# Kernel optimization log

Measured on AMD Instinct MI355X. Metric: run time of the kernel, lower is better.

The kernel has to match this reference:

```python
import jax, jax.numpy as jnp
import numpy as np

N_NODES = 50000
N_EDGES = 1600000
DIM_IN = 128
DIM_OUT = 128
EPS = 1e-10


def setup_inputs() -> dict:
    key = jax.random.key(0)
    k1, k2, k3, k4, k5 = jax.random.split(key, 5)
    feat_in = jax.random.normal(k1, (N_NODES, DIM_IN), dtype=jnp.float32)
    rows = jax.random.randint(k2, (N_EDGES,), 0, N_NODES, dtype=jnp.int32)
    cols = jax.random.randint(k3, (N_EDGES,), 0, N_NODES, dtype=jnp.int32)
    # normalized adjacency values (positive, ~1/deg scale)
    vals = jax.random.uniform(k4, (N_EDGES,), dtype=jnp.float32) / 32.0
    W = jax.random.normal(k5, (DIM_OUT, DIM_IN), dtype=jnp.float32) * 0.05
    b = jnp.zeros((DIM_OUT,), dtype=jnp.float32)
    scale = jnp.ones((DIM_OUT,), dtype=jnp.float32)
    offset = jnp.zeros((DIM_OUT,), dtype=jnp.float32)
    return {"feat_in": feat_in, "rows": rows, "cols": cols, "vals": vals,
            "W": W, "b": b, "scale": scale, "offset": offset}


def reference(feat_in, rows, cols, vals, W, b, scale, offset):
    # torch.sparse.mm(adj_norm, feat_in): gather source features, scale by
    # edge value, scatter-add into destination rows.
    msgs = vals[:, None] * feat_in[cols]                       # [E, D_in]
    feat_aggr = jax.ops.segment_sum(msgs, rows, num_segments=N_NODES)  # [N, D_in]
    # f_lin (nn.Linear): x @ W.T + b
    feat_trans = feat_aggr @ W.T + b                           # [N, D_out]
    # act = ReLU
    a = jax.nn.relu(feat_trans)
    # f_norm: per-row (feature-dim) normalization, biased variance
    mean = jnp.mean(a, axis=1, keepdims=True)
    var = jnp.mean((a - mean) ** 2, axis=1, keepdims=True) + EPS
    feat_out = (a - mean) * scale * jax.lax.rsqrt(var) + offset
    return feat_out
```

## Files before the change

kernel.cpp:

```cpp
#include <hip/hip_runtime.h>

typedef unsigned int uint;
typedef unsigned short ushort;
typedef __attribute__((ext_vector_type(8))) short short8;
typedef __attribute__((ext_vector_type(4))) float floatx4;

#define N_NODES 50000
#define N_EDGES 1600000
#define DIM 128
#define LN_EPS 1e-10f

#define ROWS_PER_BUCKET 64
#define N_BUCKETS 782
#define BUCKET_CAP 2560
#define EPB 6250
#define SB 256
#define FCB 1563
#define CAPR 76

__device__ __forceinline__ uint f2bf(float x) {
    uint u = __float_as_uint(x);
    return (u + 0x7FFFu + ((u >> 16) & 1u)) >> 16;
}

__global__ __launch_bounds__(1024) void prep(
    const float* __restrict__ feat, const float* __restrict__ W,
    const int* __restrict__ rows, const int* __restrict__ cols,
    const float* __restrict__ vals, int* __restrict__ gcnt,
    int2* __restrict__ perm, uint* __restrict__ featb_u,
    ushort* __restrict__ wbf)
{
    __shared__ int  cnt[N_BUCKETS];
    __shared__ int  gbase[N_BUCKETS];
    __shared__ int  lbase[N_BUCKETS];
    __shared__ int  csum[64];
    __shared__ uint stash[EPB];
    __shared__ int2 stageE[EPB];
    const int bx = blockIdx.x;
    const int t  = threadIdx.x;

    if (bx >= SB) {
        int cb = bx - SB;
        if (cb < FCB) {
            int i = cb * 1024 + t;
            if (i < N_NODES * DIM / 4) {
                float4 v = ((const float4*)feat)[i];
                ((uint2*)featb_u)[i] = make_uint2(
                    f2bf(v.x) | (f2bf(v.y) << 16),
                    f2bf(v.z) | (f2bf(v.w) << 16));
            }
        } else {
            for (int idx = t; idx < DIM * DIM; idx += 1024)
                wbf[idx] = (ushort)f2bf(W[idx]);
        }
        return;
    }

    for (int i = t; i < N_BUCKETS; i += 1024) cnt[i] = 0;
    __syncthreads();
    const int base = bx * EPB;
    for (int k = t; k < EPB; k += 1024) {
        int r = rows[base + k];
        int rank = atomicAdd(&cnt[r >> 6], 1);
        stash[k] = ((uint)rank << 16) | (uint)r;
    }
    __syncthreads();

    for (int i = t; i < N_BUCKETS; i += 1024) {
        int c = cnt[i];
        gbase[i] = c ? atomicAdd(&gcnt[i], c) : 0;
    }
    if (t < 64) {
        int s = 0;
        for (int j = 0; j < 13; ++j) {
            int idx = t * 13 + j;
            if (idx < N_BUCKETS) s += cnt[idx];
        }
        csum[t] = s;
    }
    __syncthreads();
    if (t == 0) {
        int s = 0;
        for (int i = 0; i < 64; ++i) { int c = csum[i]; csum[i] = s; s += c; }
    }
    __syncthreads();
    if (t < 64) {
        int run = csum[t];
        for (int j = 0; j < 13; ++j) {
            int idx = t * 13 + j;
            if (idx < N_BUCKETS) { lbase[idx] = run; run += cnt[idx]; }
        }
    }
    __syncthreads();

    for (int k = t; k < EPB; k += 1024) {
        int e = base + k;
        uint s = stash[k];
        int r = (int)(s & 0xFFFFu);
        int rank = (int)(s >> 16);
        int b = r >> 6;
        int pos = lbase[b] + rank;
        stageE[pos] = make_int2(
            (uint)cols[e] | ((uint)(r & 63) << 16) | ((uint)b << 22),
            __float_as_int(vals[e]));
    }
    __syncthreads();

    for (int j = t; j < EPB; j += 1024) {
        int2 p = stageE[j];
        uint b = ((uint)p.x) >> 22;
        int pos = gbase[b] + (j - lbase[b]);
        if (pos < BUCKET_CAP)
            perm[(size_t)b * BUCKET_CAP + pos] = p;
    }
}

__global__ __launch_bounds__(512, 6) void agg_fused(
    const int2* __restrict__ perm, const int* __restrict__ gcnt,
    const ushort* __restrict__ featb, const ushort* __restrict__ wbf,
    const float* __restrict__ bias, const float* __restrict__ scale,
    const float* __restrict__ offset, float* __restrict__ out)
{
    __shared__ int2 lists[32 * CAPR];
    ushort* rowsbuf = (ushort*)lists;
    float*  Cbuf    = (float*)lists;
    __shared__ int  lcnt[32];

    const int t = threadIdx.x;
    const int b  = blockIdx.x >> 1;
    const int lo = (blockIdx.x & 1) * 32;
    if (t < 32) lcnt[t] = 0;
    __syncthreads();

    int n = gcnt[b];
    if (n > BUCKET_CAP) n = BUCKET_CAP;
    const int2* pb = perm + (size_t)b * BUCKET_CAP;

    for (int e = t; e < n; e += 512) {
        int2 p = pb[e];
        int rl = ((p.x >> 16) & 63) - lo;
        if ((uint)rl < 32u) {
            int pos = atomicAdd(&lcnt[rl], 1);
            if (pos < CAPR)
                lists[rl * CAPR + pos] = make_int2(p.x & 0xFFFF, p.y);
        }
    }
    __syncthreads();

    const int lane = t & 63;
    const int wid  = t >> 6;
    const int rb   = wid * 4;

    float ax[4], ay[4];
    #pragma unroll
    for (int j = 0; j < 4; ++j) {
        int rl = rb + j;
        int cnt = lcnt[rl];
        if (cnt > CAPR) cnt = CAPR;
        const int2* L = &lists[rl * CAPR];
        float sx = 0.f, sy = 0.f;
        int e = 0;
        for (; e + 7 < cnt; e += 8) {
            int2 p[8]; uint g[8];
            #pragma unroll
            for (int k = 0; k < 8; ++k) p[k] = L[e + k];
            #pragma unroll
            for (int k = 0; k < 8; ++k)
                g[k] = ((const uint*)(featb + (size_t)p[k].x * DIM))[lane];
            #pragma unroll
            for (int k = 0; k < 8; ++k) {
                float v = __int_as_float(p[k].y);
                sx = fmaf(v, __uint_as_float(g[k] << 16), sx);
                sy = fmaf(v, __uint_as_float(g[k] & 0xFFFF0000u), sy);
            }
        }
        for (; e < cnt; ++e) {
            int2 p = L[e];
            uint g = ((const uint*)(featb + (size_t)p.x * DIM))[lane];
            float v = __int_as_float(p.y);
            sx = fmaf(v, __uint_as_float(g << 16), sx);
            sy = fmaf(v, __uint_as_float(g & 0xFFFF0000u), sy);
        }
        ax[j] = sx; ay[j] = sy;
    }
    __syncthreads();

    #pragma unroll
    for (int j = 0; j < 4; ++j) {
        uint pk = f2bf(ax[j]) | (f2bf(ay[j]) << 16);
        *(uint*)&rowsbuf[(rb + j) * 136 + 2 * lane] = pk;
    }
    __syncthreads();

    const int l15  = lane & 15;
    const int quad = lane >> 4;
    const int n0   = wid * 16 + l15;
    const float bb = bias[n0];

    floatx4 acc0 = {0.f, 0.f, 0.f, 0.f};
    floatx4 acc1 = {0.f, 0.f, 0.f, 0.f};
    #pragma unroll
    for (int kt = 0; kt < 4; ++kt) {
        int k0 = kt * 32 + quad * 8;
        short8 af0 = *(const short8*)&rowsbuf[l15 * 136 + k0];
        short8 af1 = *(const short8*)&rowsbuf[(l15 + 16) * 136 + k0];
        short8 bf  = *(const short8*)&wbf[n0 * DIM + k0];
        acc0 = __builtin_amdgcn_mfma_f32_16x16x32_bf16(af0, bf, acc0, 0, 0, 0);
        acc1 = __builtin_amdgcn_mfma_f32_16x16x32_bf16(af1, bf, acc1, 0, 0, 0);
    }
    __syncthreads();

    #pragma unroll
    for (int r = 0; r < 4; ++r) {
        int m = quad * 4 + r;
        Cbuf[m * 132 + n0]        = acc0[r] + bb;
        Cbuf[(m + 16) * 132 + n0] = acc1[r] + bb;
    }
    __syncthreads();

    const float sc0 = scale[lane],  sc1 = scale[lane + 64];
    const float of0 = offset[lane], of1 = offset[lane + 64];

    #pragma unroll
    for (int j = 0; j < 4; ++j) {
        int rl = rb + j;
        int r  = b * ROWS_PER_BUCKET + lo + rl;
        if (r >= N_NODES) continue;
        float A0 = fmaxf(Cbuf[rl * 132 + lane],      0.0f);
        float A1 = fmaxf(Cbuf[rl * 132 + lane + 64], 0.0f);

        float s = A0 + A1;
        #pragma unroll
        for (int off = 32; off >= 1; off >>= 1) s += __shfl_xor(s, off, 64);
        float mean = s * (1.0f / 128.0f);

        float d0 = A0 - mean, d1 = A1 - mean;
        float q = d0 * d0 + d1 * d1;
        #pragma unroll
        for (int off = 32; off >= 1; off >>= 1) q += __shfl_xor(q, off, 64);
        float rstd = rsqrtf(q * (1.0f / 128.0f) + LN_EPS);

        size_t rowp = (size_t)r * DIM;
        out[rowp + lane]      = d0 * sc0 * rstd + of0;
        out[rowp + lane + 64] = d1 * sc1 * rstd + of1;
    }
}

extern "C" void kernel_launch(void* const* d_in, const int* in_sizes, int n_in,
                              void* d_out, int out_size, void* d_ws, size_t ws_size,
                              hipStream_t stream) {
    const float* feat_in = (const float*)d_in[0];
    const int*   rows    = (const int*)d_in[1];
    const int*   cols    = (const int*)d_in[2];
    const float* vals    = (const float*)d_in[3];
    const float* W       = (const float*)d_in[4];
    const float* bias    = (const float*)d_in[5];
    const float* scale   = (const float*)d_in[6];
    const float* offset  = (const float*)d_in[7];
    float* out = (float*)d_out;

    char* p = (char*)d_ws;
    int2* perm = (int2*)p;                 p += (size_t)N_BUCKETS * BUCKET_CAP * 8;
    ushort* featb = (ushort*)p;            p += (size_t)N_NODES * DIM * 2;
    ushort* wbf = (ushort*)p;              p += DIM * DIM * 2;
    int*  gcnt = (int*)p;                  p += (size_t)(N_BUCKETS + 64) * 4;

    hipMemsetAsync(gcnt, 0, (size_t)N_BUCKETS * sizeof(int), stream);

    prep<<<SB + FCB + 1, 1024, 0, stream>>>(feat_in, W, rows, cols, vals,
                                            gcnt, perm, (uint*)featb, wbf);
    agg_fused<<<N_BUCKETS * 2, 512, 0, stream>>>(perm, gcnt, featb, wbf,
                                                 bias, scale, offset, out);
}
```

Baseline: 176.8 us.

## Split prep into convert and scatter kernels; make aggregation persistent with atomic work tickets

The feature and weight bf16 conversion moves into its own grid-stride kernel, and the bucket scatter becomes a separate kernel, where before both were packed into one mixed launch. The aggregation kernel becomes persistent: 1024 blocks pull half-bucket work items from a global atomic ticket, with occupancy raised to 8 waves per SIMD. Gather addresses are precomputed as byte offsets shifted by 8. The goals are to balance the uneven per-bucket work and to cut launch and tail imbalance. The cost is an extra kernel launch and per-item ticket atomics and barriers.

New measurement: 203.0 us. 14.8% more time.

```diff
diff --git a/kernel.cpp b/kernel.cpp
--- a/kernel.cpp
+++ b/kernel.cpp
@@ -15,20 +15,38 @@
 #define BUCKET_CAP 2560
 #define EPB 6250
 #define SB 256
-#define FCB 1563
 #define CAPR 76
+#define N_WORK (N_BUCKETS * 2)
 
 __device__ __forceinline__ uint f2bf(float x) {
     uint u = __float_as_uint(x);
     return (u + 0x7FFFu + ((u >> 16) & 1u)) >> 16;
 }
 
-__global__ __launch_bounds__(1024) void prep(
+__global__ __launch_bounds__(256) void convertk(
     const float* __restrict__ feat, const float* __restrict__ W,
+    uint* __restrict__ featb_u, ushort* __restrict__ wbf)
+{
+    const int stride = gridDim.x * 256;
+    for (int i = blockIdx.x * 256 + threadIdx.x; i < N_NODES * DIM / 4; i += stride) {
+        float4 v = ((const float4*)feat)[i];
+        ((uint2*)featb_u)[i] = make_uint2(
+            f2bf(v.x) | (f2bf(v.y) << 16),
+            f2bf(v.z) | (f2bf(v.w) << 16));
+    }
+    for (int i = blockIdx.x * 256 + threadIdx.x; i < DIM * DIM / 4; i += stride) {
+        float4 v = ((const float4*)W)[i];
+        ushort4 o;
+        o.x = (ushort)f2bf(v.x); o.y = (ushort)f2bf(v.y);
+        o.z = (ushort)f2bf(v.z); o.w = (ushort)f2bf(v.w);
+        ((ushort4*)wbf)[i] = o;
+    }
+}
+
+__global__ __launch_bounds__(1024) void scatter(
     const int* __restrict__ rows, const int* __restrict__ cols,
     const float* __restrict__ vals, int* __restrict__ gcnt,
-    int2* __restrict__ perm, uint* __restrict__ featb_u,
-    ushort* __restrict__ wbf)
+    int2* __restrict__ perm)
 {
     __shared__ int  cnt[N_BUCKETS];
     __shared__ int  gbase[N_BUCKETS];
@@ -38,23 +56,6 @@
     __shared__ int2 stageE[EPB];
     const int bx = blockIdx.x;
     const int t  = threadIdx.x;
-
-    if (bx >= SB) {
-        int cb = bx - SB;
-        if (cb < FCB) {
-            int i = cb * 1024 + t;
-            if (i < N_NODES * DIM / 4) {
-                float4 v = ((const float4*)feat)[i];
-                ((uint2*)featb_u)[i] = make_uint2(
-                    f2bf(v.x) | (f2bf(v.y) << 16),
-                    f2bf(v.z) | (f2bf(v.w) << 16));
-            }
-        } else {
-            for (int idx = t; idx < DIM * DIM; idx += 1024)
-                wbf[idx] = (ushort)f2bf(W[idx]);
-        }
-        return;
-    }
 
     for (int i = t; i < N_BUCKETS; i += 1024) cnt[i] = 0;
     __syncthreads();
@@ -115,134 +116,143 @@
     }
 }
 
-__global__ __launch_bounds__(512, 6) void agg_fused(
+__global__ __launch_bounds__(512, 8) void agg_fused(
     const int2* __restrict__ perm, const int* __restrict__ gcnt,
     const ushort* __restrict__ featb, const ushort* __restrict__ wbf,
     const float* __restrict__ bias, const float* __restrict__ scale,
-    const float* __restrict__ offset, float* __restrict__ out)
+    const float* __restrict__ offset, float* __restrict__ out,
+    int* __restrict__ ticket)
 {
     __shared__ int2 lists[32 * CAPR];
     ushort* rowsbuf = (ushort*)lists;
     float*  Cbuf    = (float*)lists;
     __shared__ int  lcnt[32];
-
-    const int t = threadIdx.x;
-    const int b  = blockIdx.x >> 1;
-    const int lo = (blockIdx.x & 1) * 32;
-    if (t < 32) lcnt[t] = 0;
-    __syncthreads();
-
-    int n = gcnt[b];
-    if (n > BUCKET_CAP) n = BUCKET_CAP;
-    const int2* pb = perm + (size_t)b * BUCKET_CAP;
-
-    for (int e = t; e < n; e += 512) {
-        int2 p = pb[e];
-        int rl = ((p.x >> 16) & 63) - lo;
-        if ((uint)rl < 32u) {
-            int pos = atomicAdd(&lcnt[rl], 1);
-            if (pos < CAPR)
-                lists[rl * CAPR + pos] = make_int2(p.x & 0xFFFF, p.y);
-        }
-    }
-    __syncthreads();
-
+    __shared__ int  curw;
+
+    const int t    = threadIdx.x;
     const int lane = t & 63;
     const int wid  = t >> 6;
     const int rb   = wid * 4;
-
-    float ax[4], ay[4];
-    #pragma unroll
-    for (int j = 0; j < 4; ++j) {
-        int rl = rb + j;
-        int cnt = lcnt[rl];
-        if (cnt > CAPR) cnt = CAPR;
-        const int2* L = &lists[rl * CAPR];
-        float sx = 0.f, sy = 0.f;
-        int e = 0;
-        for (; e + 7 < cnt; e += 8) {
-            int2 p[8]; uint g[8];
-            #pragma unroll
-            for (int k = 0; k < 8; ++k) p[k] = L[e + k];
-            #pragma unroll
-            for (int k = 0; k < 8; ++k)
-                g[k] = ((const uint*)(featb + (size_t)p[k].x * DIM))[lane];
-            #pragma unroll
-            for (int k = 0; k < 8; ++k) {
-                float v = __int_as_float(p[k].y);
-                sx = fmaf(v, __uint_as_float(g[k] << 16), sx);
-                sy = fmaf(v, __uint_as_float(g[k] & 0xFFFF0000u), sy);
-            }
-        }
-        for (; e < cnt; ++e) {
-            int2 p = L[e];
-            uint g = ((const uint*)(featb + (size_t)p.x * DIM))[lane];
-            float v = __int_as_float(p.y);
-            sx = fmaf(v, __uint_as_float(g << 16), sx);
-            sy = fmaf(v, __uint_as_float(g & 0xFFFF0000u), sy);
-        }
-        ax[j] = sx; ay[j] = sy;
-    }
-    __syncthreads();
-
-    #pragma unroll
-    for (int j = 0; j < 4; ++j) {
-        uint pk = f2bf(ax[j]) | (f2bf(ay[j]) << 16);
-        *(uint*)&rowsbuf[(rb + j) * 136 + 2 * lane] = pk;
-    }
-    __syncthreads();
-
     const int l15  = lane & 15;
     const int quad = lane >> 4;
     const int n0   = wid * 16 + l15;
-    const float bb = bias[n0];
-
-    floatx4 acc0 = {0.f, 0.f, 0.f, 0.f};
-    floatx4 acc1 = {0.f, 0.f, 0.f, 0.f};
-    #pragma unroll
-    for (int kt = 0; kt < 4; ++kt) {
-        int k0 = kt * 32 + quad * 8;
-        short8 af0 = *(const short8*)&rowsbuf[l15 * 136 + k0];
-        short8 af1 = *(const short8*)&rowsbuf[(l15 + 16) * 136 + k0];
-        short8 bf  = *(const short8*)&wbf[n0 * DIM + k0];
-        acc0 = __builtin_amdgcn_mfma_f32_16x16x32_bf16(af0, bf, acc0, 0, 0, 0);
-        acc1 = __builtin_amdgcn_mfma_f32_16x16x32_bf16(af1, bf, acc1, 0, 0, 0);
-    }
-    __syncthreads();
-
-    #pragma unroll
-    for (int r = 0; r < 4; ++r) {
-        int m = quad * 4 + r;
-        Cbuf[m * 132 + n0]        = acc0[r] + bb;
-        Cbuf[(m + 16) * 132 + n0] = acc1[r] + bb;
-    }
-    __syncthreads();
-
+
+    const float bb  = bias[n0];
     const float sc0 = scale[lane],  sc1 = scale[lane + 64];
     const float of0 = offset[lane], of1 = offset[lane + 64];
-
-    #pragma unroll
-    for (int j = 0; j < 4; ++j) {
-        int rl = rb + j;
-        int r  = b * ROWS_PER_BUCKET + lo + rl;
-        if (r >= N_NODES) continue;
-        float A0 = fmaxf(Cbuf[rl * 132 + lane],      0.0f);
-        float A1 = fmaxf(Cbuf[rl * 132 + lane + 64], 0.0f);
-
-        float s = A0 + A1;
-        #pragma unroll
-        for (int off = 32; off >= 1; off >>= 1) s += __shfl_xor(s, off, 64);
-        float mean = s * (1.0f / 128.0f);
-
-        float d0 = A0 - mean, d1 = A1 - mean;
-        float q = d0 * d0 + d1 * d1;
-        #pragma unroll
-        for (int off = 32; off >= 1; off >>= 1) q += __shfl_xor(q, off, 64);
-        float rstd = rsqrtf(q * (1.0f / 128.0f) + LN_EPS);
-
-        size_t rowp = (size_t)r * DIM;
-        out[rowp + lane]      = d0 * sc0 * rstd + of0;
-        out[rowp + lane + 64] = d1 * sc1 * rstd + of1;
+    const char* fbase = (const char*)featb;
+    const uint  lane4 = (uint)lane << 2;
+
+    while (true) {
+        __syncthreads();
+        if (t == 0) curw = atomicAdd(ticket, 1);
+        if (t < 32) lcnt[t] = 0;
+        __syncthreads();
+        const int w = curw;
+        if (w >= N_WORK) break;
+        const int b  = w >> 1;
+        const int lo = (w & 1) * 32;
+
+        int n = gcnt[b];
+        if (n > BUCKET_CAP) n = BUCKET_CAP;
+        const int2* pb = perm + (size_t)b * BUCKET_CAP;
+
+        for (int e = t; e < n; e += 512) {
+            int2 p = pb[e];
+            int rl = ((p.x >> 16) & 63) - lo;
+            if ((uint)rl < 32u) {
+                int pos = atomicAdd(&lcnt[rl], 1);
+                if (pos < CAPR)
+                    lists[rl * CAPR + pos] = make_int2((p.x & 0xFFFF) << 8, p.y);
+            }
+        }
+        __syncthreads();
+
+        float ax[4], ay[4];
+        #pragma unroll
+        for (int j = 0; j < 4; ++j) {
+            int rl = rb + j;
+            int cnt = lcnt[rl];
+            if (cnt > CAPR) cnt = CAPR;
+            const int2* L = &lists[rl * CAPR];
+            float sx = 0.f, sy = 0.f;
+            int e = 0;
+            for (; e + 7 < cnt; e += 8) {
+                int2 p[8]; uint g[8];
+                #pragma unroll
+                for (int k = 0; k < 8; ++k) p[k] = L[e + k];
+                #pragma unroll
+                for (int k = 0; k < 8; ++k)
+                    g[k] = *(const uint*)(fbase + ((uint)p[k].x + lane4));
+                #pragma unroll
+                for (int k = 0; k < 8; ++k) {
+                    float v = __int_as_float(p[k].y);
+                    sx = fmaf(v, __uint_as_float(g[k] << 16), sx);
+                    sy = fmaf(v, __uint_as_float(g[k] & 0xFFFF0000u), sy);
+                }
+            }
+            for (; e < cnt; ++e) {
+                int2 p = L[e];
+                uint g = *(const uint*)(fbase + ((uint)p.x + lane4));
+                float v = __int_as_float(p.y);
+                sx = fmaf(v, __uint_as_float(g << 16), sx);
+                sy = fmaf(v, __uint_as_float(g & 0xFFFF0000u), sy);
+            }
+            ax[j] = sx; ay[j] = sy;
+        }
+        __syncthreads();
+
+        #pragma unroll
+        for (int j = 0; j < 4; ++j) {
+            uint pk = f2bf(ax[j]) | (f2bf(ay[j]) << 16);
+            *(uint*)&rowsbuf[(rb + j) * 136 + 2 * lane] = pk;
+        }
+        __syncthreads();
+
+        floatx4 acc0 = {0.f, 0.f, 0.f, 0.f};
+        floatx4 acc1 = {0.f, 0.f, 0.f, 0.f};
+        #pragma unroll
+        for (int kt = 0; kt < 4; ++kt) {
+            int k0 = kt * 32 + quad * 8;
+            short8 af0 = *(const short8*)&rowsbuf[l15 * 136 + k0];
+            short8 af1 = *(const short8*)&rowsbuf[(l15 + 16) * 136 + k0];
+            short8 bf  = *(const short8*)&wbf[n0 * DIM + k0];
+            acc0 = __builtin_amdgcn_mfma_f32_16x16x32_bf16(af0, bf, acc0, 0, 0, 0);
+            acc1 = __builtin_amdgcn_mfma_f32_16x16x32_bf16(af1, bf, acc1, 0, 0, 0);
+        }
+        __syncthreads();
+
+        #pragma unroll
+        for (int r = 0; r < 4; ++r) {
+            int m = quad * 4 + r;
+            Cbuf[m * 132 + n0]        = acc0[r] + bb;
+            Cbuf[(m + 16) * 132 + n0] = acc1[r] + bb;
+        }
+        __syncthreads();
+
+        #pragma unroll
+        for (int j = 0; j < 4; ++j) {
+            int rl = rb + j;
+            int r  = b * ROWS_PER_BUCKET + lo + rl;
+            if (r >= N_NODES) continue;
+            float A0 = fmaxf(Cbuf[rl * 132 + lane],      0.0f);
+            float A1 = fmaxf(Cbuf[rl * 132 + lane + 64], 0.0f);
+
+            float s = A0 + A1;
+            #pragma unroll
+            for (int off = 32; off >= 1; off >>= 1) s += __shfl_xor(s, off, 64);
+            float mean = s * (1.0f / 128.0f);
+
+            float d0 = A0 - mean, d1 = A1 - mean;
+            float q = d0 * d0 + d1 * d1;
+            #pragma unroll
+            for (int off = 32; off >= 1; off >>= 1) q += __shfl_xor(q, off, 64);
+            float rstd = rsqrtf(q * (1.0f / 128.0f) + LN_EPS);
+
+            size_t rowp = (size_t)r * DIM;
+            out[rowp + lane]      = d0 * sc0 * rstd + of0;
+            out[rowp + lane + 64] = d1 * sc1 * rstd + of1;
+        }
     }
 }
 
@@ -264,11 +274,12 @@
     ushort* featb = (ushort*)p;            p += (size_t)N_NODES * DIM * 2;
     ushort* wbf = (ushort*)p;              p += DIM * DIM * 2;
     int*  gcnt = (int*)p;                  p += (size_t)(N_BUCKETS + 64) * 4;
-
-    hipMemsetAsync(gcnt, 0, (size_t)N_BUCKETS * sizeof(int), stream);
-
-    prep<<<SB + FCB + 1, 1024, 0, stream>>>(feat_in, W, rows, cols, vals,
-                                            gcnt, perm, (uint*)featb, wbf);
-    agg_fused<<<N_BUCKETS * 2, 512, 0, stream>>>(perm, gcnt, featb, wbf,
-                                                 bias, scale, offset, out);
-}
+    int*  ticket = gcnt + N_BUCKETS;
+
+    hipMemsetAsync(gcnt, 0, (size_t)(N_BUCKETS + 1) * sizeof(int), stream);
+
+    convertk<<<2048, 256, 0, stream>>>(feat_in, W, (uint*)featb, wbf);
+    scatter<<<SB, 1024, 0, stream>>>(rows, cols, vals, gcnt, perm);
+    agg_fused<<<1024, 512, 0, stream>>>(perm, gcnt, featb, wbf,
+                                        bias, scale, offset, out, ticket);
+}
```

## Bucket edges by 32 rows and remap blocks to contiguous XCD ranges

Applied to the files above, without the earlier changes.

The edge bucketing now uses 32-row buckets instead of 64. Each aggregation block reads only its own bucket, so it no longer scans and discards half of a shared 64-row bucket. Block indices are remapped so that each XCD handles a contiguous range of buckets, which should improve L2 locality for the gathered bf16 features. The gather address is precomputed as a 32-bit byte offset, and launch bounds are raised to 8 waves per SIMD. Risks include register pressure from the higher occupancy target and overflow of the smaller per-bucket capacity (1280) or the per-row list capacity, which would silently drop edges.

After: 174.9 us. About the same (-1.1%).

```diff
diff --git a/kernel.cpp b/kernel.cpp
--- a/kernel.cpp
+++ b/kernel.cpp
@@ -10,9 +10,8 @@
 #define DIM 128
 #define LN_EPS 1e-10f
 
-#define ROWS_PER_BUCKET 64
-#define N_BUCKETS 782
-#define BUCKET_CAP 2560
+#define NB2 1564
+#define CAP2 1280
 #define EPB 6250
 #define SB 256
 #define FCB 1563
@@ -30,9 +29,9 @@
     int2* __restrict__ perm, uint* __restrict__ featb_u,
     ushort* __restrict__ wbf)
 {
-    __shared__ int  cnt[N_BUCKETS];
-    __shared__ int  gbase[N_BUCKETS];
-    __shared__ int  lbase[N_BUCKETS];
+    __shared__ int  cnt[NB2];
+    __shared__ int  gbase[NB2];
+    __shared__ int  lbase[NB2];
     __shared__ int  csum[64];
     __shared__ uint stash[EPB];
     __shared__ int2 stageE[EPB];
@@ -56,25 +55,25 @@
         return;
     }
 
-    for (int i = t; i < N_BUCKETS; i += 1024) cnt[i] = 0;
+    for (int i = t; i < NB2; i += 1024) cnt[i] = 0;
     __syncthreads();
     const int base = bx * EPB;
     for (int k = t; k < EPB; k += 1024) {
         int r = rows[base + k];
-        int rank = atomicAdd(&cnt[r >> 6], 1);
+        int rank = atomicAdd(&cnt[r >> 5], 1);
         stash[k] = ((uint)rank << 16) | (uint)r;
     }
     __syncthreads();
 
-    for (int i = t; i < N_BUCKETS; i += 1024) {
+    for (int i = t; i < NB2; i += 1024) {
         int c = cnt[i];
         gbase[i] = c ? atomicAdd(&gcnt[i], c) : 0;
     }
     if (t < 64) {
         int s = 0;
-        for (int j = 0; j < 13; ++j) {
-            int idx = t * 13 + j;
-            if (idx < N_BUCKETS) s += cnt[idx];
+        for (int j = 0; j < 25; ++j) {
+            int idx = t * 25 + j;
+            if (idx < NB2) s += cnt[idx];
         }
         csum[t] = s;
     }
@@ -86,9 +85,9 @@
     __syncthreads();
     if (t < 64) {
         int run = csum[t];
-        for (int j = 0; j < 13; ++j) {
-            int idx = t * 13 + j;
-            if (idx < N_BUCKETS) { lbase[idx] = run; run += cnt[idx]; }
+        for (int j = 0; j < 25; ++j) {
+            int idx = t * 25 + j;
+            if (idx < NB2) { lbase[idx] = run; run += cnt[idx]; }
         }
     }
     __syncthreads();
@@ -98,24 +97,24 @@
         uint s = stash[k];
         int r = (int)(s & 0xFFFFu);
         int rank = (int)(s >> 16);
-        int b = r >> 6;
+        int b = r >> 5;
         int pos = lbase[b] + rank;
         stageE[pos] = make_int2(
-            (uint)cols[e] | ((uint)(r & 63) << 16) | ((uint)b << 22),
+            (uint)cols[e] | ((uint)(r & 31) << 16) | ((uint)b << 21),
             __float_as_int(vals[e]));
     }
     __syncthreads();
 
     for (int j = t; j < EPB; j += 1024) {
         int2 p = stageE[j];
-        uint b = ((uint)p.x) >> 22;
+        uint b = ((uint)p.x) >> 21;
         int pos = gbase[b] + (j - lbase[b]);
-        if (pos < BUCKET_CAP)
-            perm[(size_t)b * BUCKET_CAP + pos] = p;
-    }
-}
-
-__global__ __launch_bounds__(512, 6) void agg_fused(
+        if (pos < CAP2)
+            perm[(size_t)b * CAP2 + pos] = p;
+    }
+}
+
+__global__ __launch_bounds__(512, 8) void agg_fused(
     const int2* __restrict__ perm, const int* __restrict__ gcnt,
     const ushort* __restrict__ featb, const ushort* __restrict__ wbf,
     const float* __restrict__ bias, const float* __restrict__ scale,
@@ -127,29 +126,32 @@
     __shared__ int  lcnt[32];
 
     const int t = threadIdx.x;
-    const int b  = blockIdx.x >> 1;
-    const int lo = (blockIdx.x & 1) * 32;
+
+    const int q = NB2 >> 3, rr = NB2 & 7;
+    const int xcd = blockIdx.x & 7, within = blockIdx.x >> 3;
+    const int hb = (xcd < rr ? xcd * (q + 1) : rr * (q + 1) + (xcd - rr) * q) + within;
+
     if (t < 32) lcnt[t] = 0;
     __syncthreads();
 
-    int n = gcnt[b];
-    if (n > BUCKET_CAP) n = BUCKET_CAP;
-    const int2* pb = perm + (size_t)b * BUCKET_CAP;
+    int n = gcnt[hb];
+    if (n > CAP2) n = CAP2;
+    const int2* pb = perm + (size_t)hb * CAP2;
 
     for (int e = t; e < n; e += 512) {
         int2 p = pb[e];
-        int rl = ((p.x >> 16) & 63) - lo;
-        if ((uint)rl < 32u) {
-            int pos = atomicAdd(&lcnt[rl], 1);
-            if (pos < CAPR)
-                lists[rl * CAPR + pos] = make_int2(p.x & 0xFFFF, p.y);
-        }
+        int rl = (p.x >> 16) & 31;
+        int pos = atomicAdd(&lcnt[rl], 1);
+        if (pos < CAPR)
+            lists[rl * CAPR + pos] = make_int2((p.x & 0xFFFF) << 8, p.y);
     }
     __syncthreads();
 
     const int lane = t & 63;
     const int wid  = t >> 6;
     const int rb   = wid * 4;
+    const char* fbase = (const char*)featb;
+    const uint  lane4 = (uint)lane << 2;
 
     float ax[4], ay[4];
     #pragma unroll
@@ -166,7 +168,7 @@
             for (int k = 0; k < 8; ++k) p[k] = L[e + k];
             #pragma unroll
             for (int k = 0; k < 8; ++k)
-                g[k] = ((const uint*)(featb + (size_t)p[k].x * DIM))[lane];
+                g[k] = *(const uint*)(fbase + ((uint)p[k].x + lane4));
             #pragma unroll
             for (int k = 0; k < 8; ++k) {
                 float v = __int_as_float(p[k].y);
@@ -176,7 +178,7 @@
         }
         for (; e < cnt; ++e) {
             int2 p = L[e];
-            uint g = ((const uint*)(featb + (size_t)p.x * DIM))[lane];
+            uint g = *(const uint*)(fbase + ((uint)p.x + lane4));
             float v = __int_as_float(p.y);
             sx = fmaf(v, __uint_as_float(g << 16), sx);
             sy = fmaf(v, __uint_as_float(g & 0xFFFF0000u), sy);
@@ -224,7 +226,7 @@
     #pragma unroll
     for (int j = 0; j < 4; ++j) {
         int rl = rb + j;
-        int r  = b * ROWS_PER_BUCKET + lo + rl;
+        int r  = hb * 32 + rl;
         if (r >= N_NODES) continue;
         float A0 = fmaxf(Cbuf[rl * 132 + lane],      0.0f);
         float A1 = fmaxf(Cbuf[rl * 132 + lane + 64], 0.0f);
@@ -235,10 +237,10 @@
         float mean = s * (1.0f / 128.0f);
 
         float d0 = A0 - mean, d1 = A1 - mean;
-        float q = d0 * d0 + d1 * d1;
+        float q2 = d0 * d0 + d1 * d1;
         #pragma unroll
-        for (int off = 32; off >= 1; off >>= 1) q += __shfl_xor(q, off, 64);
-        float rstd = rsqrtf(q * (1.0f / 128.0f) + LN_EPS);
+        for (int off = 32; off >= 1; off >>= 1) q2 += __shfl_xor(q2, off, 64);
+        float rstd = rsqrtf(q2 * (1.0f / 128.0f) + LN_EPS);
 
         size_t rowp = (size_t)r * DIM;
         out[rowp + lane]      = d0 * sc0 * rstd + of0;
@@ -260,15 +262,15 @@
     float* out = (float*)d_out;
 
     char* p = (char*)d_ws;
-    int2* perm = (int2*)p;                 p += (size_t)N_BUCKETS * BUCKET_CAP * 8;
+    int2* perm = (int2*)p;                 p += (size_t)NB2 * CAP2 * 8;
     ushort* featb = (ushort*)p;            p += (size_t)N_NODES * DIM * 2;
     ushort* wbf = (ushort*)p;              p += DIM * DIM * 2;
-    int*  gcnt = (int*)p;                  p += (size_t)(N_BUCKETS + 64) * 4;
-
-    hipMemsetAsync(gcnt, 0, (size_t)N_BUCKETS * sizeof(int), stream);
+    int*  gcnt = (int*)p;                  p += (size_t)(NB2 + 64) * 4;
+
+    hipMemsetAsync(gcnt, 0, (size_t)NB2 * sizeof(int), stream);
 
     prep<<<SB + FCB + 1, 1024, 0, stream>>>(feat_in, W, rows, cols, vals,
                                             gcnt, perm, (uint*)featb, wbf);
-    agg_fused<<<N_BUCKETS * 2, 512, 0, stream>>>(perm, gcnt, featb, wbf,
-                                                 bias, scale, offset, out);
-}
+    agg_fused<<<NB2, 512, 0, stream>>>(perm, gcnt, featb, wbf,
+                                       bias, scale, offset, out);
+}
```
